# Optimization experiments

Measured on AMD Instinct MI355X. Metric: run time of the kernel, lower is better.

## Reference

```python
import jax, jax.numpy as jnp
import numpy as np

SQRT_2PI = (2.0 * 3.1415926) ** 0.5  # matches pi literal in original code


def setup_inputs() -> dict:
    key = jax.random.key(0)
    ks = jax.random.split(key, 8)
    B, L, A, KNN, K = 4, 1024, 5, 32, 16
    X = jax.random.normal(ks[0], (B, L, A, 3), dtype=jnp.float32)
    E_idx = jax.random.randint(ks[1], (B, L, KNN), 0, L)
    mask_atoms = jnp.ones((B, L, A), dtype=jnp.float32)
    mask_attend = jnp.ones((B, L, KNN), dtype=jnp.float32)
    means = jax.random.normal(ks[2], (K,), dtype=jnp.float32)
    stds = jax.random.normal(ks[3], (K,), dtype=jnp.float32)
    mul = jax.random.normal(ks[4], (A * A,), dtype=jnp.float32)
    bias = jax.random.normal(ks[5], (A * A,), dtype=jnp.float32)
    return {"X": X, "E_idx": E_idx, "mask_atoms": mask_atoms,
            "mask_attend": mask_attend, "means": means, "stds": stds,
            "mul": mul, "bias": bias}


def reference(X, E_idx, mask_atoms, mask_attend, means, stds, mul, bias):
    B, L, A, _ = X.shape
    K = means.shape[0]
    b_idx = jnp.arange(B)[:, None, None]
    # gather neighbor coords: [B, L, k, A, 3]
    neighbors_X = X.reshape(B, L, A * 3)[b_idx, E_idx].reshape(B, L, -1, A, 3)
    # pairwise distances neighbor-atom i vs center-atom j: [B, L, k, A, A]
    delta = neighbors_X[:, :, :, :, None, :] - X[:, :, None, None, :, :]
    D = jnp.linalg.norm(delta, axis=-1)
    # per-edge-type affine
    mul_e = mul.reshape(A, A)
    bias_e = bias.reshape(A, A)
    x = mul_e * D + bias_e
    # atom-pair mask from gathered neighbor atom masks
    mask_na = mask_atoms[b_idx, E_idx]  # [B, L, k, A]
    mask_pair = mask_na[:, :, :, None, :] * mask_na[:, :, :, :, None]
    x = x * mask_pair
    # gaussian RBF expansion over K channels
    std = jnp.abs(stds) + 0.01
    z = (x[..., None] - means) / std  # [B, L, k, A, A, K]
    gbf = jnp.exp(-0.5 * z * z) / (SQRT_2PI * std)
    gbf = gbf.reshape(B, L, -1, A * A * K)
    return gbf * mask_attend[..., None]
```

## Files before the change

kernel.cpp:

```cpp
#include <hip/hip_runtime.h>

constexpr int A_DIM  = 5;
constexpr int PAIRS  = 25;
constexpr int KNN    = 32;
constexpr int L_DIM  = 1024;
constexpr int B_DIM  = 4;
constexpr float INV_SQRT_2PI = 0.39894228f;

typedef float f32x4 __attribute__((ext_vector_type(4)));

__global__ __launch_bounds__(64) void setup_consts(
    const float* __restrict__ means, const float* __restrict__ stds,
    float* __restrict__ ws)
{
    const int k = threadIdx.x;
    if (k < 16) {
        const float sd  = fabsf(stds[k]) + 0.01f;
        const float inv = __builtin_amdgcn_rcpf(sd);
        ws[k]      = means[k];
        ws[16 + k] = inv;
        ws[32 + k] = inv * INV_SQRT_2PI;
    }
}

__global__ __launch_bounds__(256) void gauss_rbf_kernel(
    const float*  __restrict__ X,
    const int*    __restrict__ E_idx,
    const float*  __restrict__ mask_atoms,
    const float*  __restrict__ mask_attend,
    const float*  __restrict__ mul,
    const float*  __restrict__ bias,
    const f32x4*  __restrict__ cst,
    f32x4*        __restrict__ out4)
{
    const int tid = threadIdx.x;
    const int c   = tid & 3;
    const f32x4 mu4 = cst[c];
    const f32x4 iv4 = cst[4 + c];
    const f32x4 co4 = cst[8 + c];

    unsigned fbase = blockIdx.x * 1024u + (unsigned)tid;

#pragma unroll
    for (int u = 0; u < 4; ++u) {
        const unsigned fidx = fbase + u * 256u;
        const unsigned q    = fidx >> 2;
        const unsigned e    = q / PAIRS;
        const int      pair = (int)(q - e * PAIRS);
        const int      i    = pair / A_DIM;
        const int      j    = pair - i * A_DIM;

        const unsigned bl = e >> 5;
        const unsigned b  = bl >> 10;
        const int      n  = E_idx[e];
        const unsigned bn = (b << 10) | (unsigned)n;

        const float* xn = X + ((size_t)bn * A_DIM + i) * 3;
        const float* xc = X + ((size_t)bl * A_DIM + j) * 3;
        const float dx = xn[0] - xc[0];
        const float dy = xn[1] - xc[1];
        const float dz = xn[2] - xc[2];
        const float D  = sqrtf(dx * dx + dy * dy + dz * dz);

        const float mi = mask_atoms[(size_t)bn * A_DIM + i];
        const float mj = mask_atoms[(size_t)bn * A_DIM + j];

        const float x   = (mul[pair] * D + bias[pair]) * (mi * mj);
        const float att = mask_attend[e];

        f32x4 o;
        {
            const float z0 = (x - mu4.x) * iv4.x;
            const float z1 = (x - mu4.y) * iv4.y;
            const float z2 = (x - mu4.z) * iv4.z;
            const float z3 = (x - mu4.w) * iv4.w;
            o.x = (co4.x * att) * __expf(-0.5f * z0 * z0);
            o.y = (co4.y * att) * __expf(-0.5f * z1 * z1);
            o.z = (co4.z * att) * __expf(-0.5f * z2 * z2);
            o.w = (co4.w * att) * __expf(-0.5f * z3 * z3);
        }

        __builtin_nontemporal_store(o, &out4[fidx]);
    }
}

extern "C" void kernel_launch(void* const* d_in, const int* in_sizes, int n_in,
                              void* d_out, int out_size, void* d_ws, size_t ws_size,
                              hipStream_t stream) {
    const float* X           = (const float*)d_in[0];
    const int*   E_idx       = (const int*)  d_in[1];
    const float* mask_atoms  = (const float*)d_in[2];
    const float* mask_attend = (const float*)d_in[3];
    const float* means       = (const float*)d_in[4];
    const float* stds        = (const float*)d_in[5];
    const float* mul         = (const float*)d_in[6];
    const float* bias        = (const float*)d_in[7];
    float*       ws          = (float*)d_ws;
    f32x4*       out4        = (f32x4*)d_out;

    setup_consts<<<1, 64, 0, stream>>>(means, stds, ws);

    const int total_f4 = B_DIM * L_DIM * KNN * PAIRS * 4;
    const int grid     = total_f4 / 1024;

    gauss_rbf_kernel<<<grid, 256, 0, stream>>>(
        X, E_idx, mask_atoms, mask_attend, mul, bias,
        (const f32x4*)ws, out4);
}
```

Measured before the change: 46.19 us.

## Compute per-pair distances once per block into LDS, then expand RBF

The kernel is split into two phases per block of 64 edges. First each atom pair's affine-masked distance is computed once and stored in shared memory. Then threads read it back to emit the 16 Gaussian channels as float4 stores. This removes the 4x redundant gather, sqrt and index math the old version did for every float4 of the same pair. The cost is a __syncthreads, LDS traffic, fewer blocks and a divergent first phase where only part of the threads are busy.

```diff
diff --git a/kernel.cpp b/kernel.cpp
--- a/kernel.cpp
+++ b/kernel.cpp
@@ -5,6 +5,9 @@
 constexpr int KNN    = 32;
 constexpr int L_DIM  = 1024;
 constexpr int B_DIM  = 4;
+constexpr int EPB    = 64;
+constexpr int QPB    = EPB * PAIRS;
+constexpr int F4PB   = QPB * 4;
 constexpr float INV_SQRT_2PI = 0.39894228f;
 
 typedef float f32x4 __attribute__((ext_vector_type(4)));
@@ -33,54 +36,69 @@
     const f32x4*  __restrict__ cst,
     f32x4*        __restrict__ out4)
 {
-    const int tid = threadIdx.x;
-    const int c   = tid & 3;
+    __shared__ float x_lds[QPB];
+    __shared__ float att_lds[EPB];
+
+    const int      tid = threadIdx.x;
+    const unsigned blk = blockIdx.x;
+    const unsigned e0  = blk * EPB;
+
+    const int   c   = tid & 3;
     const f32x4 mu4 = cst[c];
     const f32x4 iv4 = cst[4 + c];
     const f32x4 co4 = cst[8 + c];
 
-    unsigned fbase = blockIdx.x * 1024u + (unsigned)tid;
+    if (tid < EPB) att_lds[tid] = mask_attend[e0 + tid];
 
 #pragma unroll
-    for (int u = 0; u < 4; ++u) {
-        const unsigned fidx = fbase + u * 256u;
-        const unsigned q    = fidx >> 2;
-        const unsigned e    = q / PAIRS;
-        const int      pair = (int)(q - e * PAIRS);
-        const int      i    = pair / A_DIM;
-        const int      j    = pair - i * A_DIM;
+    for (int w = 0; w < 7; ++w) {
+        const int s = tid + 256 * w;
+        if (s < QPB) {
+            const unsigned g    = (unsigned)s / PAIRS;
+            const int      pair = s - (int)g * PAIRS;
+            const int      i    = pair / A_DIM;
+            const int      j    = pair - i * A_DIM;
 
-        const unsigned bl = e >> 5;
-        const unsigned b  = bl >> 10;
-        const int      n  = E_idx[e];
-        const unsigned bn = (b << 10) | (unsigned)n;
+            const unsigned e  = e0 + g;
+            const unsigned bl = e >> 5;
+            const unsigned b  = bl >> 10;
+            const int      n  = E_idx[e];
+            const unsigned bn = (b << 10) | (unsigned)n;
 
-        const float* xn = X + ((size_t)bn * A_DIM + i) * 3;
-        const float* xc = X + ((size_t)bl * A_DIM + j) * 3;
-        const float dx = xn[0] - xc[0];
-        const float dy = xn[1] - xc[1];
-        const float dz = xn[2] - xc[2];
-        const float D  = sqrtf(dx * dx + dy * dy + dz * dz);
+            const float* xn = X + ((size_t)bn * A_DIM + i) * 3;
+            const float* xc = X + ((size_t)bl * A_DIM + j) * 3;
+            const float dx = xn[0] - xc[0];
+            const float dy = xn[1] - xc[1];
+            const float dz = xn[2] - xc[2];
+            const float D  = sqrtf(dx * dx + dy * dy + dz * dz);
 
-        const float mi = mask_atoms[(size_t)bn * A_DIM + i];
-        const float mj = mask_atoms[(size_t)bn * A_DIM + j];
+            const float mi = mask_atoms[(size_t)bn * A_DIM + i];
+            const float mj = mask_atoms[(size_t)bn * A_DIM + j];
 
-        const float x   = (mul[pair] * D + bias[pair]) * (mi * mj);
-        const float att = mask_attend[e];
+            x_lds[s] = (mul[pair] * D + bias[pair]) * (mi * mj);
+        }
+    }
+    __syncthreads();
 
+    const int tq = tid >> 2;
+#pragma unroll 5
+    for (int u = 0; u < 25; ++u) {
+        const int      q   = tq + 64 * u;
+        const unsigned g   = (unsigned)q / PAIRS;
+        const float    x   = x_lds[q];
+        const float    att = att_lds[g];
+
+        const float z0 = (x - mu4.x) * iv4.x;
+        const float z1 = (x - mu4.y) * iv4.y;
+        const float z2 = (x - mu4.z) * iv4.z;
+        const float z3 = (x - mu4.w) * iv4.w;
         f32x4 o;
-        {
-            const float z0 = (x - mu4.x) * iv4.x;
-            const float z1 = (x - mu4.y) * iv4.y;
-            const float z2 = (x - mu4.z) * iv4.z;
-            const float z3 = (x - mu4.w) * iv4.w;
-            o.x = (co4.x * att) * __expf(-0.5f * z0 * z0);
-            o.y = (co4.y * att) * __expf(-0.5f * z1 * z1);
-            o.z = (co4.z * att) * __expf(-0.5f * z2 * z2);
-            o.w = (co4.w * att) * __expf(-0.5f * z3 * z3);
-        }
+        o.x = (co4.x * att) * __expf(-0.5f * z0 * z0);
+        o.y = (co4.y * att) * __expf(-0.5f * z1 * z1);
+        o.z = (co4.z * att) * __expf(-0.5f * z2 * z2);
+        o.w = (co4.w * att) * __expf(-0.5f * z3 * z3);
 
-        __builtin_nontemporal_store(o, &out4[fidx]);
+        __builtin_nontemporal_store(o, &out4[(size_t)blk * F4PB + tid + 256 * u]);
     }
 }
 
@@ -100,8 +118,8 @@
 
     setup_consts<<<1, 64, 0, stream>>>(means, stds, ws);
 
-    const int total_f4 = B_DIM * L_DIM * KNN * PAIRS * 4;
-    const int grid     = total_f4 / 1024;
+    const int n_edges = B_DIM * L_DIM * KNN;
+    const int grid    = n_edges / EPB;
 
     gauss_rbf_kernel<<<grid, 256, 0, stream>>>(
         X, E_idx, mask_atoms, mask_attend, mul, bias,
```

Result: slower. 52.85 us (+14.4%).

## Precompute per-edge affine distances in a separate pass before RBF write

Applied to the files above, without the earlier changes.

Splits the work into two kernels. The first computes the 25 masked affine pair distances for each edge, loading the neighbor and center coordinates once per edge. The second streams these values back and writes the Gaussian expansion. This removes redundant gathers and sqrt work in the store-heavy kernel, but adds a workspace write and read of about 13 MB, an extra launch dependency, and relies on the workspace being large enough.

```diff
diff --git a/kernel.cpp b/kernel.cpp
--- a/kernel.cpp
+++ b/kernel.cpp
@@ -1,84 +1,96 @@
 #include <hip/hip_runtime.h>
 
-constexpr int A_DIM  = 5;
-constexpr int PAIRS  = 25;
-constexpr int KNN    = 32;
-constexpr int L_DIM  = 1024;
-constexpr int B_DIM  = 4;
+constexpr int A_DIM   = 5;
+constexpr int PAIRS   = 25;
+constexpr int KNN     = 32;
+constexpr int L_DIM   = 1024;
+constexpr int B_DIM   = 4;
+constexpr int N_EDGES = B_DIM * L_DIM * KNN;
 constexpr float INV_SQRT_2PI = 0.39894228f;
 
 typedef float f32x4 __attribute__((ext_vector_type(4)));
 
-__global__ __launch_bounds__(64) void setup_consts(
-    const float* __restrict__ means, const float* __restrict__ stds,
-    float* __restrict__ ws)
+
+__global__ __launch_bounds__(256) void edge_x_kernel(
+    const float* __restrict__ X,
+    const int*   __restrict__ E_idx,
+    const float* __restrict__ mask_atoms,
+    const float* __restrict__ means,
+    const float* __restrict__ stds,
+    const float* __restrict__ mul,
+    const float* __restrict__ bias,
+    float*       __restrict__ ws)
 {
-    const int k = threadIdx.x;
-    if (k < 16) {
+    if (blockIdx.x == 0 && threadIdx.x < 16) {
+        const int   k   = threadIdx.x;
         const float sd  = fabsf(stds[k]) + 0.01f;
         const float inv = __builtin_amdgcn_rcpf(sd);
         ws[k]      = means[k];
         ws[16 + k] = inv;
         ws[32 + k] = inv * INV_SQRT_2PI;
     }
+
+    const unsigned e  = blockIdx.x * 256u + threadIdx.x;
+    const unsigned bl = e >> 5;
+    const unsigned b  = bl >> 10;
+    const int      n  = E_idx[e];
+    const unsigned bn = (b << 10) | (unsigned)n;
+
+    const float* Xn = X + (size_t)bn * 15;
+    const float* Xc = X + (size_t)bl * 15;
+    float xn[15], xc[15], m[5];
+#pragma unroll
+    for (int t = 0; t < 15; ++t) { xn[t] = Xn[t]; xc[t] = Xc[t]; }
+#pragma unroll
+    for (int t = 0; t < 5; ++t) m[t] = mask_atoms[(size_t)bn * 5 + t];
+
+    float* xo = ws + 48 + (size_t)e * PAIRS;
+#pragma unroll
+    for (int i = 0; i < 5; ++i) {
+#pragma unroll
+        for (int j = 0; j < 5; ++j) {
+            const float dx = xn[3*i]   - xc[3*j];
+            const float dy = xn[3*i+1] - xc[3*j+1];
+            const float dz = xn[3*i+2] - xc[3*j+2];
+            const float D  = sqrtf(dx*dx + dy*dy + dz*dz);
+            const int   p  = i * 5 + j;
+            xo[p] = (mul[p] * D + bias[p]) * (m[i] * m[j]);
+        }
+    }
 }
 
-__global__ __launch_bounds__(256) void gauss_rbf_kernel(
-    const float*  __restrict__ X,
-    const int*    __restrict__ E_idx,
-    const float*  __restrict__ mask_atoms,
-    const float*  __restrict__ mask_attend,
-    const float*  __restrict__ mul,
-    const float*  __restrict__ bias,
-    const f32x4*  __restrict__ cst,
-    f32x4*        __restrict__ out4)
+__global__ __launch_bounds__(256) void rbf_write_kernel(
+    const float* __restrict__ ws,
+    const float* __restrict__ mask_attend,
+    f32x4*       __restrict__ out4)
 {
     const int tid = threadIdx.x;
     const int c   = tid & 3;
+    const f32x4* cst = (const f32x4*)ws;
     const f32x4 mu4 = cst[c];
     const f32x4 iv4 = cst[4 + c];
     const f32x4 co4 = cst[8 + c];
+    const float* xw = ws + 48;
 
-    unsigned fbase = blockIdx.x * 1024u + (unsigned)tid;
+    const unsigned fbase = blockIdx.x * 1024u + (unsigned)tid;
 
 #pragma unroll
     for (int u = 0; u < 4; ++u) {
-        const unsigned fidx = fbase + u * 256u;
+        const unsigned fidx = fbase + 256u * u;
         const unsigned q    = fidx >> 2;
         const unsigned e    = q / PAIRS;
-        const int      pair = (int)(q - e * PAIRS);
-        const int      i    = pair / A_DIM;
-        const int      j    = pair - i * A_DIM;
+        const float    x    = xw[q];
+        const float    att  = mask_attend[e];
 
-        const unsigned bl = e >> 5;
-        const unsigned b  = bl >> 10;
-        const int      n  = E_idx[e];
-        const unsigned bn = (b << 10) | (unsigned)n;
-
-        const float* xn = X + ((size_t)bn * A_DIM + i) * 3;
-        const float* xc = X + ((size_t)bl * A_DIM + j) * 3;
-        const float dx = xn[0] - xc[0];
-        const float dy = xn[1] - xc[1];
-        const float dz = xn[2] - xc[2];
-        const float D  = sqrtf(dx * dx + dy * dy + dz * dz);
-
-        const float mi = mask_atoms[(size_t)bn * A_DIM + i];
-        const float mj = mask_atoms[(size_t)bn * A_DIM + j];
-
-        const float x   = (mul[pair] * D + bias[pair]) * (mi * mj);
-        const float att = mask_attend[e];
-
+        const float z0 = (x - mu4.x) * iv4.x;
+        const float z1 = (x - mu4.y) * iv4.y;
+        const float z2 = (x - mu4.z) * iv4.z;
+        const float z3 = (x - mu4.w) * iv4.w;
         f32x4 o;
-        {
-            const float z0 = (x - mu4.x) * iv4.x;
-            const float z1 = (x - mu4.y) * iv4.y;
-            const float z2 = (x - mu4.z) * iv4.z;
-            const float z3 = (x - mu4.w) * iv4.w;
-            o.x = (co4.x * att) * __expf(-0.5f * z0 * z0);
-            o.y = (co4.y * att) * __expf(-0.5f * z1 * z1);
-            o.z = (co4.z * att) * __expf(-0.5f * z2 * z2);
-            o.w = (co4.w * att) * __expf(-0.5f * z3 * z3);
-        }
+        o.x = (co4.x * att) * __expf(-0.5f * z0 * z0);
+        o.y = (co4.y * att) * __expf(-0.5f * z1 * z1);
+        o.z = (co4.z * att) * __expf(-0.5f * z2 * z2);
+        o.w = (co4.w * att) * __expf(-0.5f * z3 * z3);
 
         __builtin_nontemporal_store(o, &out4[fidx]);
     }
@@ -98,12 +110,10 @@
     float*       ws          = (float*)d_ws;
     f32x4*       out4        = (f32x4*)d_out;
 
-    setup_consts<<<1, 64, 0, stream>>>(means, stds, ws);
+    edge_x_kernel<<<N_EDGES / 256, 256, 0, stream>>>(
+        X, E_idx, mask_atoms, means, stds, mul, bias, ws);
 
-    const int total_f4 = B_DIM * L_DIM * KNN * PAIRS * 4;
-    const int grid     = total_f4 / 1024;
-
-    gauss_rbf_kernel<<<grid, 256, 0, stream>>>(
-        X, E_idx, mask_atoms, mask_attend, mul, bias,
-        (const f32x4*)ws, out4);
+    const int total_f4 = N_EDGES * PAIRS * 4;
+    rbf_write_kernel<<<total_f4 / 1024, 256, 0, stream>>>(
+        ws, mask_attend, out4);
 }
```

New measurement: 50.92 us. +10.2%, slower.

## Fold constant setup into main kernel and give each thread more output work

Applied to the files above, without the earlier changes.

Removes the separate setup_consts launch: each thread now computes its own means, reciprocal stds and normalisation constants directly from the inputs. The main kernel also goes from 4 to 32 float4 outputs per thread, each wave owning a contiguous 2048-float4 span, so the grid has 8x fewer blocks. This cuts one kernel launch plus per-block setup overhead. In exchange there is less parallelism per launch and some redundant per-thread constant computation.

```diff
diff --git a/kernel.cpp b/kernel.cpp
--- a/kernel.cpp
+++ b/kernel.cpp
@@ -1,49 +1,51 @@
 #include <hip/hip_runtime.h>
 
-constexpr int A_DIM  = 5;
-constexpr int PAIRS  = 25;
-constexpr int KNN    = 32;
-constexpr int L_DIM  = 1024;
-constexpr int B_DIM  = 4;
+constexpr int A_DIM   = 5;
+constexpr int PAIRS   = 25;
+constexpr int KNN     = 32;
+constexpr int L_DIM   = 1024;
+constexpr int B_DIM   = 4;
+constexpr int N_EDGES = B_DIM * L_DIM * KNN;
+constexpr int TOTAL_F4 = N_EDGES * PAIRS * 4;
+constexpr int F4_PER_THREAD = 32;
+constexpr int F4_PER_BLOCK  = 256 * F4_PER_THREAD;
 constexpr float INV_SQRT_2PI = 0.39894228f;
 
 typedef float f32x4 __attribute__((ext_vector_type(4)));
 
-__global__ __launch_bounds__(64) void setup_consts(
-    const float* __restrict__ means, const float* __restrict__ stds,
-    float* __restrict__ ws)
+__global__ __launch_bounds__(256) void gauss_rbf_kernel(
+    const float* __restrict__ X,
+    const int*   __restrict__ E_idx,
+    const float* __restrict__ mask_atoms,
+    const float* __restrict__ mask_attend,
+    const float* __restrict__ means,
+    const float* __restrict__ stds,
+    const float* __restrict__ mul,
+    const float* __restrict__ bias,
+    f32x4*       __restrict__ out4)
 {
-    const int k = threadIdx.x;
-    if (k < 16) {
+    const int tid  = threadIdx.x;
+    const int lane = tid & 63;
+    const int wave = tid >> 6;
+    const int c    = lane & 3;
+
+    f32x4 mu4, iv4, co4;
+#pragma unroll
+    for (int t = 0; t < 4; ++t) {
+        const int   k   = c * 4 + t;
         const float sd  = fabsf(stds[k]) + 0.01f;
         const float inv = __builtin_amdgcn_rcpf(sd);
-        ws[k]      = means[k];
-        ws[16 + k] = inv;
-        ws[32 + k] = inv * INV_SQRT_2PI;
+        mu4[t] = means[k];
+        iv4[t] = inv;
+        co4[t] = inv * INV_SQRT_2PI;
     }
-}
 
-__global__ __launch_bounds__(256) void gauss_rbf_kernel(
-    const float*  __restrict__ X,
-    const int*    __restrict__ E_idx,
-    const float*  __restrict__ mask_atoms,
-    const float*  __restrict__ mask_attend,
-    const float*  __restrict__ mul,
-    const float*  __restrict__ bias,
-    const f32x4*  __restrict__ cst,
-    f32x4*        __restrict__ out4)
-{
-    const int tid = threadIdx.x;
-    const int c   = tid & 3;
-    const f32x4 mu4 = cst[c];
-    const f32x4 iv4 = cst[4 + c];
-    const f32x4 co4 = cst[8 + c];
+    const unsigned wbase = blockIdx.x * (unsigned)F4_PER_BLOCK
+                         + (unsigned)wave * 2048u + (unsigned)lane;
 
-    unsigned fbase = blockIdx.x * 1024u + (unsigned)tid;
-
-#pragma unroll
-    for (int u = 0; u < 4; ++u) {
-        const unsigned fidx = fbase + u * 256u;
+#pragma unroll 4
+    for (int it = 0; it < F4_PER_THREAD; ++it) {
+        const unsigned fidx = wbase + (unsigned)it * 64u;
         const unsigned q    = fidx >> 2;
         const unsigned e    = q / PAIRS;
         const int      pair = (int)(q - e * PAIRS);
@@ -68,17 +70,15 @@
         const float x   = (mul[pair] * D + bias[pair]) * (mi * mj);
         const float att = mask_attend[e];
 
+        const float z0 = (x - mu4.x) * iv4.x;
+        const float z1 = (x - mu4.y) * iv4.y;
+        const float z2 = (x - mu4.z) * iv4.z;
+        const float z3 = (x - mu4.w) * iv4.w;
         f32x4 o;
-        {
-            const float z0 = (x - mu4.x) * iv4.x;
-            const float z1 = (x - mu4.y) * iv4.y;
-            const float z2 = (x - mu4.z) * iv4.z;
-            const float z3 = (x - mu4.w) * iv4.w;
-            o.x = (co4.x * att) * __expf(-0.5f * z0 * z0);
-            o.y = (co4.y * att) * __expf(-0.5f * z1 * z1);
-            o.z = (co4.z * att) * __expf(-0.5f * z2 * z2);
-            o.w = (co4.w * att) * __expf(-0.5f * z3 * z3);
-        }
+        o.x = (co4.x * att) * __expf(-0.5f * z0 * z0);
+        o.y = (co4.y * att) * __expf(-0.5f * z1 * z1);
+        o.z = (co4.z * att) * __expf(-0.5f * z2 * z2);
+        o.w = (co4.w * att) * __expf(-0.5f * z3 * z3);
 
         __builtin_nontemporal_store(o, &out4[fidx]);
     }
@@ -95,15 +95,10 @@
     const float* stds        = (const float*)d_in[5];
     const float* mul         = (const float*)d_in[6];
     const float* bias        = (const float*)d_in[7];
-    float*       ws          = (float*)d_ws;
     f32x4*       out4        = (f32x4*)d_out;
 
-    setup_consts<<<1, 64, 0, stream>>>(means, stds, ws);
-
-    const int total_f4 = B_DIM * L_DIM * KNN * PAIRS * 4;
-    const int grid     = total_f4 / 1024;
+    const int grid = TOTAL_F4 / F4_PER_BLOCK;
 
     gauss_rbf_kernel<<<grid, 256, 0, stream>>>(
-        X, E_idx, mask_atoms, mask_attend, mul, bias,
-        (const f32x4*)ws, out4);
+        X, E_idx, mask_atoms, mask_attend, means, stds, mul, bias, out4);
 }
```

Result: slower. 47.61 us (+3.1%).
